# Kernel tuning notes

Measured on AMD Instinct MI355X. Metric: run time of the kernel, lower is better.

## Reference

```python
import jax, jax.numpy as jnp
import numpy as np

MARGIN = 0.0
BINS = 10
ALPHA = 0.75
N = 16777216  # 2**24 pairs


def setup_inputs() -> dict:
    key = jax.random.key(0)
    k1, k2, k3 = jax.random.split(key, 3)
    output1 = jax.random.normal(k1, (N,), dtype=jnp.float32)
    output2 = jax.random.normal(k2, (N,), dtype=jnp.float32)
    target = jax.random.randint(k3, (N,), 0, 2, dtype=jnp.int64)
    return {"output1": output1, "output2": output2, "target": target}


def reference(output1, output2, target):
    dtype = output1.dtype
    t = target.astype(dtype)
    diff = output1 - output2
    # MarginRankingLoss(reduction='none'): max(0, -target*(x1-x2) + margin)
    loss = jnp.maximum(0.0, -t * diff + MARGIN)
    # gradient-norm proxy g in (0,1)
    expected_sign = 2.0 * t - 1.0
    g = jax.nn.sigmoid(-diff * expected_sign + MARGIN)
    g_norm = jnp.abs(g)
    edges = jnp.arange(BINS + 1, dtype=dtype) / BINS
    # histogram over BINS bins (fixed small loop over bins, vectorized over N)
    counts = jnp.stack([
        jnp.sum((g_norm >= edges[i]) & (g_norm < edges[i + 1]))
        for i in range(BINS)
    ]).astype(dtype)
    tot = jnp.clip(counts, 1.0)
    w = tot ** (-ALPHA)  # per-bin weight; constant wrt g in the original (.item() detaches)
    w = jax.lax.stop_gradient(w)
    bin_idx = jnp.clip(jnp.floor(g * BINS).astype(jnp.int32), 0, BINS - 1)
    sample_weights = w[bin_idx]
    return jnp.mean(loss * sample_weights)
```

## Files before the change

### kernel.cpp

```cpp
#include <hip/hip_runtime.h>

#define BINS 10
#define ALPHA 0.75f

constexpr int NB    = 2048;
constexpr int NT    = 256;
constexpr int ITERS = 8;
constexpr int NT2   = 1024;

__device__ __constant__ float LTH[9] = {
    2.19722458f,  1.38629436f,  0.847297861f, 0.405465108f, 0.0f,
   -0.405465108f, -0.847297861f, -1.38629436f, -2.19722458f};

#define GHM_PROC(AX, BX, TX) do {                                    \
    float diff = (AX) - (BX);                                        \
    float nd   = -diff;                                              \
    bool  tt   = (TX) != 0;                                          \
    float u    = tt ? diff : nd;                                     \
    float loss = tt ? fmaxf(nd, 0.0f) : 0.0f;                        \
    cls[0] += loss;                                                  \
    _Pragma("unroll")                                                \
    for (int k = 1; k < BINS; ++k) {                                 \
      bool p = (u <= LTH[k - 1]);                                    \
      cls[k] += p ? loss : 0.0f;                                     \
      cnt[k] += (unsigned int)p;                                     \
    }                                                                \
  } while (0)

__global__ __launch_bounds__(NT, 4) void ghm_pass1(
    const float* __restrict__ o1f, const float* __restrict__ o2f,
    const int* __restrict__ tgt, float* __restrict__ lsum_part,
    unsigned int* __restrict__ cnt_part, int n)
{
  const float4* o1 = reinterpret_cast<const float4*>(o1f);
  const float4* o2 = reinterpret_cast<const float4*>(o2f);
  const int4*   tg = reinterpret_cast<const int4*>(tgt);

  float        cls[BINS];
  unsigned int cnt[BINS];
#pragma unroll
  for (int b = 0; b < BINS; ++b) { cls[b] = 0.0f; cnt[b] = 0u; }

  if (n == NB * NT * ITERS * 4 && gridDim.x == NB) {
    const int base = blockIdx.x * (NT * ITERS) + threadIdx.x;
    float4 av[ITERS], bv[ITERS];
    int4   tv[ITERS];
#pragma unroll
    for (int k = 0; k < ITERS; ++k) {
      av[k] = o1[base + k * NT];
      bv[k] = o2[base + k * NT];
      tv[k] = tg[base + k * NT];
    }
#pragma unroll
    for (int k = 0; k < ITERS; ++k) {
      GHM_PROC(av[k].x, bv[k].x, tv[k].x);
      GHM_PROC(av[k].y, bv[k].y, tv[k].y);
      GHM_PROC(av[k].z, bv[k].z, tv[k].z);
      GHM_PROC(av[k].w, bv[k].w, tv[k].w);
    }
  } else {
    const int tid = blockIdx.x * NT + threadIdx.x;
    const int stride = gridDim.x * NT;
    const int n4 = n >> 2;
    for (int i = tid; i < n4; i += stride) {
      float4 a  = o1[i];
      float4 bb = o2[i];
      int4   t  = tg[i];
      GHM_PROC(a.x, bb.x, t.x);
      GHM_PROC(a.y, bb.y, t.y);
      GHM_PROC(a.z, bb.z, t.z);
      GHM_PROC(a.w, bb.w, t.w);
    }
    if (tid == 0) {
      for (int i = n4 * 4; i < n; ++i) GHM_PROC(o1f[i], o2f[i], tgt[i]);
    }
  }

  const int lane = threadIdx.x & 63;
  const int wv   = threadIdx.x >> 6;
  __shared__ float        s_ls[NT / 64][BINS];
  __shared__ unsigned int s_c [NT / 64][BINS];
#pragma unroll
  for (int b = 0; b < BINS; ++b) {
    float v = cls[b];
    unsigned int cv = cnt[b];
#pragma unroll
    for (int off = 32; off >= 1; off >>= 1) {
      v  += __shfl_down(v, off, 64);
      cv += __shfl_down(cv, off, 64);
    }
    if (lane == 0) { s_ls[wv][b] = v; s_c[wv][b] = cv; }
  }
  __syncthreads();
  if (threadIdx.x < BINS) {
    float v = 0.0f; unsigned int cv = 0u;
#pragma unroll
    for (int w = 0; w < NT / 64; ++w) { v += s_ls[w][threadIdx.x]; cv += s_c[w][threadIdx.x]; }
    lsum_part[blockIdx.x * BINS + threadIdx.x] = v;
    cnt_part [blockIdx.x * BINS + threadIdx.x] = cv;
  }
}

__global__ __launch_bounds__(NT2) void ghm_pass2(
    const float* __restrict__ lsum_part, const unsigned int* __restrict__ cnt_part,
    float* __restrict__ out, int nparts, int n)
{
  double             cls[BINS];
  unsigned long long cc [BINS];
#pragma unroll
  for (int b = 0; b < BINS; ++b) { cls[b] = 0.0; cc[b] = 0ull; }

  for (int i = threadIdx.x; i < nparts; i += NT2) {
#pragma unroll
    for (int b = 0; b < BINS; ++b) {
      cls[b] += (double)lsum_part[i * BINS + b];
      cc[b]  += (unsigned long long)cnt_part[i * BINS + b];
    }
  }

  const int lane = threadIdx.x & 63;
  const int wv   = threadIdx.x >> 6;
  __shared__ double             s_ls[NT2 / 64][BINS];
  __shared__ unsigned long long s_c [NT2 / 64][BINS];
#pragma unroll
  for (int b = 0; b < BINS; ++b) {
    double v = cls[b];
    unsigned long long cv = cc[b];
#pragma unroll
    for (int off = 32; off >= 1; off >>= 1) {
      v  += __shfl_down(v, off, 64);
      cv += __shfl_down(cv, off, 64);
    }
    if (lane == 0) { s_ls[wv][b] = v; s_c[wv][b] = cv; }
  }
  __syncthreads();
  if (threadIdx.x == 0) {
    double             CLS[BINS + 1];
    unsigned long long CC [BINS + 1];
#pragma unroll
    for (int b = 0; b < BINS; ++b) {
      double lv = 0.0; unsigned long long cv = 0ull;
#pragma unroll
      for (int w = 0; w < NT2 / 64; ++w) { lv += s_ls[w][b]; cv += s_c[w][b]; }
      CLS[b] = lv; CC[b] = cv;
    }
    CLS[BINS] = 0.0; CC[BINS] = 0ull;
    CC[0] = (unsigned long long)n;

    double total = 0.0;
#pragma unroll
    for (int b = 0; b < BINS; ++b) {
      double lsb             = CLS[b] - CLS[b + 1];
      unsigned long long cb  = CC[b] - CC[b + 1];
      float cf  = (float)cb;
      float tot = fmaxf(cf, 1.0f);
      float wgt = powf(tot, -ALPHA);
      total += lsb * (double)wgt;
    }
    out[0] = (float)(total / (double)n);
  }
}

extern "C" void kernel_launch(void* const* d_in, const int* in_sizes, int n_in,
                              void* d_out, int out_size, void* d_ws, size_t ws_size,
                              hipStream_t stream) {
  const float* o1  = (const float*)d_in[0];
  const float* o2  = (const float*)d_in[1];
  const int*   tgt = (const int*)d_in[2];
  float* out = (float*)d_out;
  const int n = in_sizes[0];

  int nb = NB;
  size_t need = (size_t)nb * BINS * (sizeof(float) + sizeof(unsigned int));
  while (nb > 1 && need > ws_size) { nb >>= 1; need >>= 1; }
  float* lsum_part = (float*)d_ws;
  unsigned int* cnt_part = (unsigned int*)((char*)d_ws + (size_t)nb * BINS * sizeof(float));

  ghm_pass1<<<nb, NT, 0, stream>>>(o1, o2, tgt, lsum_part, cnt_part, n);
  ghm_pass2<<<1, NT2, 0, stream>>>(lsum_part, cnt_part, out, nb, n);
}
```

Before: 215.8 us.

## Software-pipeline pass1 loads with depth-2 prefetch and transpose partial layout

Replaces the load-all-then-compute scheme in pass1 with a rolling two-deep register prefetch. A sched_barrier keeps the compiler from hoisting all loads, which cuts register pressure. The launch_bounds occupancy hint is dropped. The per-block partial sums are stored bin-major so pass2 reads them coalesced across threads. This trades the memory-level parallelism of eight in-flight loads per thread for lower VGPR use and more interleaving of memory and compute.

```diff
diff --git a/kernel.cpp b/kernel.cpp
--- a/kernel.cpp
+++ b/kernel.cpp
@@ -27,7 +27,14 @@
     }                                                                \
   } while (0)
 
-__global__ __launch_bounds__(NT, 4) void ghm_pass1(
+#define GHM_PROC4(AV, BV, TV) do {                                   \
+    GHM_PROC((AV).x, (BV).x, (TV).x);                                \
+    GHM_PROC((AV).y, (BV).y, (TV).y);                                \
+    GHM_PROC((AV).z, (BV).z, (TV).z);                                \
+    GHM_PROC((AV).w, (BV).w, (TV).w);                                \
+  } while (0)
+
+__global__ __launch_bounds__(NT) void ghm_pass1(
     const float* __restrict__ o1f, const float* __restrict__ o2f,
     const int* __restrict__ tgt, float* __restrict__ lsum_part,
     unsigned int* __restrict__ cnt_part, int n)
@@ -43,21 +50,20 @@
 
   if (n == NB * NT * ITERS * 4 && gridDim.x == NB) {
     const int base = blockIdx.x * (NT * ITERS) + threadIdx.x;
-    float4 av[ITERS], bv[ITERS];
-    int4   tv[ITERS];
+    float4 a0 = o1[base];      float4 b0 = o2[base];      int4 t0 = tg[base];
+    float4 a1 = o1[base + NT]; float4 b1 = o2[base + NT]; int4 t1 = tg[base + NT];
 #pragma unroll
-    for (int k = 0; k < ITERS; ++k) {
-      av[k] = o1[base + k * NT];
-      bv[k] = o2[base + k * NT];
-      tv[k] = tg[base + k * NT];
+    for (int k = 0; k < ITERS - 2; ++k) {
+      float4 a2 = o1[base + (k + 2) * NT];
+      float4 b2 = o2[base + (k + 2) * NT];
+      int4   t2 = tg[base + (k + 2) * NT];
+      __builtin_amdgcn_sched_barrier(0);
+      GHM_PROC4(a0, b0, t0);
+      a0 = a1; b0 = b1; t0 = t1;
+      a1 = a2; b1 = b2; t1 = t2;
     }
-#pragma unroll
-    for (int k = 0; k < ITERS; ++k) {
-      GHM_PROC(av[k].x, bv[k].x, tv[k].x);
-      GHM_PROC(av[k].y, bv[k].y, tv[k].y);
-      GHM_PROC(av[k].z, bv[k].z, tv[k].z);
-      GHM_PROC(av[k].w, bv[k].w, tv[k].w);
-    }
+    GHM_PROC4(a0, b0, t0);
+    GHM_PROC4(a1, b1, t1);
   } else {
     const int tid = blockIdx.x * NT + threadIdx.x;
     const int stride = gridDim.x * NT;
@@ -66,10 +72,7 @@
       float4 a  = o1[i];
       float4 bb = o2[i];
       int4   t  = tg[i];
-      GHM_PROC(a.x, bb.x, t.x);
-      GHM_PROC(a.y, bb.y, t.y);
-      GHM_PROC(a.z, bb.z, t.z);
-      GHM_PROC(a.w, bb.w, t.w);
+      GHM_PROC4(a, bb, t);
     }
     if (tid == 0) {
       for (int i = n4 * 4; i < n; ++i) GHM_PROC(o1f[i], o2f[i], tgt[i]);
@@ -96,8 +99,8 @@
     float v = 0.0f; unsigned int cv = 0u;
 #pragma unroll
     for (int w = 0; w < NT / 64; ++w) { v += s_ls[w][threadIdx.x]; cv += s_c[w][threadIdx.x]; }
-    lsum_part[blockIdx.x * BINS + threadIdx.x] = v;
-    cnt_part [blockIdx.x * BINS + threadIdx.x] = cv;
+    lsum_part[threadIdx.x * gridDim.x + blockIdx.x] = v;
+    cnt_part [threadIdx.x * gridDim.x + blockIdx.x] = cv;
   }
 }
 
@@ -113,8 +116,8 @@
   for (int i = threadIdx.x; i < nparts; i += NT2) {
 #pragma unroll
     for (int b = 0; b < BINS; ++b) {
-      cls[b] += (double)lsum_part[i * BINS + b];
-      cc[b]  += (unsigned long long)cnt_part[i * BINS + b];
+      cls[b] += (double)lsum_part[b * nparts + i];
+      cc[b]  += (unsigned long long)cnt_part[b * nparts + i];
     }
   }
 
@@ -150,8 +153,8 @@
     double total = 0.0;
 #pragma unroll
     for (int b = 0; b < BINS; ++b) {
-      double lsb             = CLS[b] - CLS[b + 1];
-      unsigned long long cb  = CC[b] - CC[b + 1];
+      double lsb            = CLS[b] - CLS[b + 1];
+      unsigned long long cb = CC[b] - CC[b + 1];
       float cf  = (float)cb;
       float tot = fmaxf(cf, 1.0f);
       float wgt = powf(tot, -ALPHA);
```

Result: slower. 220.7 us (+2.2%).
